# Kernel tuning notes

Measured on AMD Instinct MI355X. Metric: run time of the kernel, lower is better.

The kernel has to match this reference:

```python
import jax, jax.numpy as jnp
import numpy as np

DN = ('NCHW', 'OIHW', 'NCHW')
THRESHOLD = 20   # Broyden iterations (hardcoded in the torch forward)


def conv(x, k):
    return jax.lax.conv_general_dilated(x, k, (1, 1), 'SAME', dimension_numbers=DN)


def _matvec(Us, VTs, v):
    # (-I + Us @ VTs) v ; Us [B,D,K], VTs [B,K,D], v [B,D]
    return -v + jnp.einsum('bdk,bk->bd', Us, jnp.einsum('bkd,bd->bk', VTs, v))


def _rmatvec(Us, VTs, v):
    # v^T (-I + Us @ VTs)
    return -v + jnp.einsum('bk,bkd->bd', jnp.einsum('bd,bdk->bk', v, Us), VTs)


def broyden_solve(g, x0, threshold):
    """Broyden's method with low-rank inverse-Jacobian updates (J^{-1} = -I + Us VTs),
    returning the iterate with the lowest residual norm (as in the DEQ broyden solver)."""
    B, D = x0.shape
    x, gx = x0, g(x0)
    Us = jnp.zeros((B, D, threshold), x0.dtype)
    VTs = jnp.zeros((B, threshold, D), x0.dtype)
    best_x, best_obj = x, jnp.linalg.norm(gx)
    update = gx  # -(-I) gx with empty low-rank part
    for k in range(threshold):
        x_new = x + update
        gx_new = g(x_new)
        dx, dgx = x_new - x, gx_new - gx
        vT = _rmatvec(Us, VTs, dx)                       # [B,D]
        denom = jnp.einsum('bd,bd->b', vT, dgx)[:, None]
        denom = jnp.where(jnp.abs(denom) < 1e-9, 1e-9, denom)
        u = (dx - _matvec(Us, VTs, dgx)) / denom
        Us = Us.at[:, :, k].set(u)
        VTs = VTs.at[:, k, :].set(vT)
        x, gx = x_new, gx_new
        obj = jnp.linalg.norm(gx)
        best_x = jnp.where(obj < best_obj, x, best_x)
        best_obj = jnp.minimum(obj, best_obj)
        update = -_matvec(Us, VTs, gx)
    return best_x


def setup_inputs() -> dict:
    key = jax.random.key(0)
    k1, k2, k3, k4 = jax.random.split(key, 4)
    B, Cin, Cout, H, W = 16, 64, 128, 32, 32
    x = jax.random.normal(k1, (B, Cin, H, W), jnp.float32)
    # small-norm A so relu(conv(z,A)+...) is a contraction -> equilibrium exists
    A = jax.random.normal(k2, (Cout, Cout, 3, 3), jnp.float32) * 0.02
    U = jax.random.normal(k3, (Cout, Cin, 3, 3), jnp.float32) * 0.05
    b = jax.random.normal(k4, (1, Cout, 1, 1), jnp.float32) * 0.1
    return {'x': x, 'A': A, 'U': U, 'b': b}


def reference(x, A, U, b):
    B, _, H, W = x.shape
    Cout = A.shape[0]
    D = Cout * H * W
    ux = conv(x, U) + b  # input injection, constant over iterations

    def g(zvec):  # residual g(z) = relu(Wz + Ux + b) - z, flattened
        z = zvec.reshape(B, Cout, H, W)
        return (jax.nn.relu(conv(z, A) + ux) - z).reshape(B, D)

    z0 = jnp.zeros((B, D), x.dtype)
    zstar = broyden_solve(g, z0, THRESHOLD).reshape(B, Cout, H, W)
    # final recompute with the equilibrium (the torch code re-runs linear+nonlin)
    zn = jax.nn.relu(conv(zstar, A) + ux)
    return zn
```

## Files before the change

### kernel.cpp

```cpp
#include <hip/hip_runtime.h>

#define NB    16
#define CIN_  64
#define COUT_ 128
#define PLANE_ 1024
#define DDIM  (COUT_*PLANE_)
#define BDTOT ((size_t)NB*DDIM)
#define KMAX  20
#define SMAX  16
#define SEG   (DDIM / SMAX)
#define GRP8  (SEG / 8)
#define CBLK  128
#define PADC  8

typedef short  bfrag __attribute__((ext_vector_type(8)));
typedef float  ffrag __attribute__((ext_vector_type(4)));

__device__ __forceinline__ float bf2f(unsigned short h) {
    return __uint_as_float(((unsigned int)h) << 16);
}
__device__ __forceinline__ unsigned short f2bf(float f) {
    unsigned int u = __float_as_uint(f);
    u = (u + 0x7FFFu + ((u >> 16) & 1u)) >> 16;
    return (unsigned short)u;
}
__device__ __forceinline__ void bf2x(unsigned int w, float& lo, float& hi) {
    lo = __uint_as_float(w << 16);
    hi = __uint_as_float(w & 0xffff0000u);
}
__device__ __forceinline__ unsigned int packbf(float lo, float hi) {
    return ((unsigned int)f2bf(hi) << 16) | (unsigned int)f2bf(lo);
}
__device__ __forceinline__ void ub4(ushort4 a, float* f) {
    f[0] = bf2f(a.x); f[1] = bf2f(a.y); f[2] = bf2f(a.z); f[3] = bf2f(a.w);
}
__device__ __forceinline__ ushort4 pk4(const float* f) {
    ushort4 r; r.x = f2bf(f[0]); r.y = f2bf(f[1]); r.z = f2bf(f[2]); r.w = f2bf(f[3]);
    return r;
}
__device__ __forceinline__ void ub8(uint4 a, float* f) {
    bf2x(a.x, f[0], f[1]); bf2x(a.y, f[2], f[3]);
    bf2x(a.z, f[4], f[5]); bf2x(a.w, f[6], f[7]);
}
__device__ __forceinline__ float wred(float v) {
    #pragma unroll
    for (int m = 32; m > 0; m >>= 1) v += __shfl_xor(v, m, 64);
    return v;
}

template<int CIN>
__device__ __forceinline__ void conv_stage_lds(
    const unsigned short* __restrict__ zsrc, unsigned short* lds,
    int hrow, int n, int tid)
{
    const int CP = CIN + PADC;
    const int CH8 = CIN / 8;
    for (int idx = tid; idx < 102 * CH8; idx += 256) {
        int slot = idx / CH8, chunk = idx - slot * CH8;
        int row = slot / 34, pxm = slot - row * 34;
        int h = hrow + row - 1, w = pxm - 1;
        uint4 val = {0u, 0u, 0u, 0u};
        if ((unsigned)h < 32u && (unsigned)w < 32u)
            val = *(const uint4*)(zsrc + ((size_t)n * PLANE_ + h * 32 + w) * CIN + chunk * 8);
        *(uint4*)(lds + (slot)*CP + chunk * 8) = val;
    }
    __syncthreads();
}

template<int CIN>
__device__ __forceinline__ void conv_compute_lds(
    const unsigned short* lds, const unsigned short* __restrict__ Wt,
    int co_base, int col, int quad, ffrag accs[4])
{
    const int CP = CIN + PADC;
    #pragma unroll
    for (int cb = 0; cb < CIN; cb += 32) {
        #pragma unroll
        for (int tap = 0; tap < 9; ++tap) {
            const int dh = tap / 3, dwi = tap % 3;
            const unsigned short* wr0 =
                Wt + ((size_t)tap * COUT_ + co_base + col) * CIN + quad * 8 + cb;
            bfrag a0 = *(const bfrag*)(wr0);
            bfrag a1 = *(const bfrag*)(wr0 + 16 * CIN);
            bfrag b0 = *(const bfrag*)(lds + (dh * 34 + col + dwi) * CP + cb + quad * 8);
            bfrag b1 = *(const bfrag*)(lds + (dh * 34 + col + 16 + dwi) * CP + cb + quad * 8);
            accs[0] = __builtin_amdgcn_mfma_f32_16x16x32_bf16(a0, b0, accs[0], 0, 0, 0);
            accs[1] = __builtin_amdgcn_mfma_f32_16x16x32_bf16(a0, b1, accs[1], 0, 0, 0);
            accs[2] = __builtin_amdgcn_mfma_f32_16x16x32_bf16(a1, b0, accs[2], 0, 0, 0);
            accs[3] = __builtin_amdgcn_mfma_f32_16x16x32_bf16(a1, b1, accs[3], 0, 0, 0);
        }
    }
}

__global__ __launch_bounds__(256) void conv_ux_kernel(
    const unsigned short* __restrict__ xinb, const unsigned short* __restrict__ WU,
    const float* __restrict__ bias, float* __restrict__ ux,
    unsigned short* __restrict__ uxb)
{
    __shared__ unsigned short lds[3 * 34 * (CIN_ + PADC)];
    const int hrow = blockIdx.x, n = blockIdx.y;
    const int tid = threadIdx.x, lane = tid & 63, wv = tid >> 6;
    const int col = lane & 15, quad = lane >> 4;
    conv_stage_lds<CIN_>(xinb, lds, hrow, n, tid);
    ffrag accs[4] = {{0.f,0.f,0.f,0.f},{0.f,0.f,0.f,0.f},{0.f,0.f,0.f,0.f},{0.f,0.f,0.f,0.f}};
    conv_compute_lds<CIN_>(lds, WU, wv * 32, col, quad, accs);
    #pragma unroll
    for (int f = 0; f < 4; ++f) {
        const int mt = f >> 1, nt = f & 1;
        const int co = wv * 32 + mt * 16 + quad * 4;
        const int px = hrow * 32 + nt * 16 + col;
        const size_t o = ((size_t)n * PLANE_ + px) * COUT_ + co;
        float4 bv = *(const float4*)(bias + co);
        float r[4] = {accs[f][0] + bv.x, accs[f][1] + bv.y, accs[f][2] + bv.z, accs[f][3] + bv.w};
        *(float4*)(ux + o) = make_float4(r[0], r[1], r[2], r[3]);
        *(ushort4*)(uxb + o) = pk4(r);
    }
}

__global__ __launch_bounds__(256) void conv_bro_kernel(
    const unsigned short* __restrict__ zb, const unsigned short* __restrict__ WA,
    const unsigned short* __restrict__ uxb, const float* __restrict__ xv,
    unsigned short* gxb,
    const unsigned short* __restrict__ updb,
    unsigned short* __restrict__ dgxb,
    float* __restrict__ cparts)
{
    __shared__ unsigned short lds[3 * 34 * (COUT_ + PADC)];
    const int hrow = blockIdx.x, n = blockIdx.y;
    const int tid = threadIdx.x, lane = tid & 63, wv = tid >> 6;
    const int col = lane & 15, quad = lane >> 4;
    conv_stage_lds<COUT_>(zb, lds, hrow, n, tid);
    ffrag accs[4] = {{0.f,0.f,0.f,0.f},{0.f,0.f,0.f,0.f},{0.f,0.f,0.f,0.f},{0.f,0.f,0.f,0.f}};
    conv_compute_lds<COUT_>(lds, WA, wv * 32, col, quad, accs);

    float s0 = 0.f, s1 = 0.f, s2 = 0.f, s3 = 0.f, s4 = 0.f, s5 = 0.f;
    #pragma unroll
    for (int f = 0; f < 4; ++f) {
        const int mt = f >> 1, nt = f & 1;
        const int co = wv * 32 + mt * 16 + quad * 4;
        const int px = hrow * 32 + nt * 16 + col;
        const size_t o = ((size_t)n * PLANE_ + px) * COUT_ + co;
        float uxv[4], gov[4], udv[4];
        ub4(*(const ushort4*)(uxb + o), uxv);
        ub4(*(const ushort4*)(gxb + o), gov);
        ub4(*(const ushort4*)(updb + o), udv);
        float4 xc = *(const float4*)(xv + o);
        float g[4], dgv[4];
        #pragma unroll
        for (int r = 0; r < 4; ++r) {
            float tv = accs[f][r] + uxv[r];
            tv = tv > 0.f ? tv : 0.f;
            g[r] = tv - (&xc.x)[r];
            dgv[r] = g[r] - gov[r];
            s0 += udv[r] * dgv[r];
            s1 += udv[r] * g[r];
            s2 += g[r] * g[r];
            s3 += udv[r] * udv[r];
            s4 += dgv[r] * dgv[r];
            s5 += dgv[r] * g[r];
        }
        *(ushort4*)(gxb + o)  = pk4(g);
        *(ushort4*)(dgxb + o) = pk4(dgv);
    }
    s0 = wred(s0); s1 = wred(s1); s2 = wred(s2);
    s3 = wred(s3); s4 = wred(s4); s5 = wred(s5);
    if (lane == 0) {
        const int blk = hrow * 4 + wv;
        cparts[((size_t)0 * NB + n) * CBLK + blk] = s0;
        cparts[((size_t)1 * NB + n) * CBLK + blk] = s1;
        cparts[((size_t)2 * NB + n) * CBLK + blk] = s2;
        cparts[((size_t)3 * NB + n) * CBLK + blk] = s3;
        cparts[((size_t)4 * NB + n) * CBLK + blk] = s4;
        cparts[((size_t)5 * NB + n) * CBLK + blk] = s5;
    }
}

__global__ __launch_bounds__(256) void conv_final_kernel(
    const unsigned short* __restrict__ bestzb, const unsigned short* __restrict__ WA,
    const float* __restrict__ ux, float* __restrict__ out)
{
    __shared__ unsigned short lds[3 * 34 * (COUT_ + PADC)];
    const int hrow = blockIdx.x, n = blockIdx.y;
    const int tid = threadIdx.x, lane = tid & 63, wv = tid >> 6;
    const int col = lane & 15, quad = lane >> 4;
    conv_stage_lds<COUT_>(bestzb, lds, hrow, n, tid);
    ffrag accs[4] = {{0.f,0.f,0.f,0.f},{0.f,0.f,0.f,0.f},{0.f,0.f,0.f,0.f},{0.f,0.f,0.f,0.f}};
    conv_compute_lds<COUT_>(lds, WA, wv * 32, col, quad, accs);
    #pragma unroll
    for (int f = 0; f < 4; ++f) {
        const int mt = f >> 1, nt = f & 1;
        const int co = wv * 32 + mt * 16 + quad * 4;
        const int px = hrow * 32 + nt * 16 + col;
        const size_t o = ((size_t)n * PLANE_ + px) * COUT_ + co;
        float4 uv = *(const float4*)(ux + o);
        #pragma unroll
        for (int r = 0; r < 4; ++r) {
            float t = accs[f][r] + (&uv.x)[r];
            out[((size_t)n * COUT_ + co + r) * PLANE_ + px] = t > 0.f ? t : 0.f;
        }
    }
}

#define NWA (9 * 128 * 128)
#define NWU (9 * 128 * 64)
__global__ __launch_bounds__(256) void prep_w_kernel(
    const float* __restrict__ A, const float* __restrict__ U,
    unsigned short* __restrict__ WA, unsigned short* __restrict__ WU)
{
    int idx = blockIdx.x * 256 + threadIdx.x;
    if (idx < NWA) {
        int tap = idx / (128 * 128), r = idx % (128 * 128);
        int co = r >> 7, ci = r & 127;
        WA[idx] = f2bf(A[(co * 128 + ci) * 9 + tap]);
    } else if (idx < NWA + NWU) {
        int j = idx - NWA;
        int tap = j / (128 * 64), r = j % (128 * 64);
        int co = r >> 6, ci = r & 63;
        WU[j] = f2bf(U[(co * 64 + ci) * 9 + tap]);
    }
}

__global__ __launch_bounds__(256) void prep_xin_kernel(
    const float* __restrict__ x, unsigned short* __restrict__ xb)
{
    int idx = blockIdx.x * 256 + threadIdx.x;
    int n = idx >> 16, r = idx & 65535;
    int px = r >> 6, ci = r & 63;
    xb[idx] = f2bf(x[(n * 64 + ci) * 1024 + px]);
}

__global__ __launch_bounds__(256) void fill0_kernel(float* __restrict__ a)
{
    size_t i = ((size_t)blockIdx.x * 256 + threadIdx.x) * 4;
    *(float4*)(a + i) = make_float4(0.f, 0.f, 0.f, 0.f);
}

__global__ __launch_bounds__(256) void ew_init_kernel(
    const float* __restrict__ ux, unsigned short* __restrict__ gxb,
    unsigned short* __restrict__ updb, float* __restrict__ xv,
    unsigned short* __restrict__ zb, float* __restrict__ objinit)
{
    const int tid = threadIdx.x;
    size_t i = ((size_t)blockIdx.x * 256 + tid) * 8;
    float rr[8];
    float ob = 0.f;
    #pragma unroll
    for (int h = 0; h < 2; ++h) {
        float4 u = *(const float4*)(ux + i + h * 4);
        #pragma unroll
        for (int r = 0; r < 4; ++r) {
            float v = (&u.x)[r];
            v = v > 0.f ? v : 0.f;
            v = bf2f(f2bf(v));
            rr[h*4+r] = v;
            ob += v * v;
        }
    }
    uint4 m = {packbf(rr[0],rr[1]), packbf(rr[2],rr[3]), packbf(rr[4],rr[5]), packbf(rr[6],rr[7])};
    *(uint4*)(gxb  + i) = m;
    *(uint4*)(updb + i) = m;
    *(uint4*)(zb   + i) = m;
    #pragma unroll
    for (int h = 0; h < 2; ++h)
        *(float4*)(xv + i + h * 4) = make_float4(rr[h*4+0], rr[h*4+1], rr[h*4+2], rr[h*4+3]);

    __shared__ float so[256];
    so[tid] = ob;
    __syncthreads();
    for (int s = 128; s > 0; s >>= 1) {
        if (tid < s) so[tid] += so[tid + s];
        __syncthreads();
    }
    if (tid == 0) objinit[blockIdx.x] = so[0];
}

__global__ __launch_bounds__(256) void dots_kernel(
    const unsigned short* __restrict__ Us, const unsigned short* __restrict__ VTs,
    const unsigned short* __restrict__ dgxb,
    float* __restrict__ tparts, int k)
{
    const int b = blockIdx.x, y = blockIdx.y, s = blockIdx.z;
    const int tid = threadIdx.x;
    const size_t segbase = (size_t)b * DDIM + (size_t)s * SEG;
    const unsigned short* M = (y < k) ? (VTs + (size_t)y * BDTOT)
                                      : (Us + (size_t)(y - k) * BDTOT);
    const uint4* m8 = (const uint4*)(M + segbase);
    const uint4* d8 = (const uint4*)(dgxb + segbase);
    float s0 = 0.f;
    #pragma unroll
    for (int it = 0; it < GRP8 / 256; ++it) {
        int g = it * 256 + tid;
        float mv[8], dv[8];
        ub8(m8[g], mv); ub8(d8[g], dv);
        #pragma unroll
        for (int j = 0; j < 8; ++j) s0 = fmaf(mv[j], dv[j], s0);
    }
    __shared__ float r0[256];
    r0[tid] = s0;
    __syncthreads();
    for (int st = 128; st > 0; st >>= 1) {
        if (tid < st) r0[tid] += r0[tid + st];
        __syncthreads();
    }
    if (tid == 0) tparts[((size_t)y * NB + b) * SMAX + s] = r0[0];
}

__global__ __launch_bounds__(256) void pass2_kernel(
    unsigned short* __restrict__ Us, unsigned short* __restrict__ VTs,
    unsigned short* updb,
    const unsigned short* __restrict__ dgxb, const unsigned short* __restrict__ gxb,
    float* xv, unsigned short* __restrict__ zb, unsigned short* __restrict__ bestzb,
    const float* __restrict__ tparts, const float* __restrict__ cparts,
    const float* __restrict__ objinit,
    const float* __restrict__ parr_r, float* __restrict__ parr_w,
    const float* __restrict__ tp_r, float* __restrict__ tp_w,
    const float* __restrict__ hp_r, float* __restrict__ hp_w,
    float* __restrict__ UU, float* __restrict__ obj_arr, int k)
{
    const int b = blockIdx.y;
    const int bx = blockIdx.x;
    const int tid = threadIdx.x;
    const int lane = tid & 63, wv = tid >> 6;

    __shared__ float sq[KMAX], st[KMAX], sp[KMAX], sr[KMAX], sh[KMAX], UUk[KMAX];
    __shared__ float sS[5];
    __shared__ float sden, sc, sflag, sobj, srk;
    __shared__ float red[256];

    {
        float o = 0.f;
        const float* OB = cparts + (size_t)2 * NB * CBLK;
        for (int j = tid; j < NB * CBLK; j += 256) o += OB[j];
        red[tid] = o;
        __syncthreads();
        for (int s = 128; s > 0; s >>= 1) {
            if (tid < s) red[tid] += red[tid + s];
            __syncthreads();
        }
        if (tid == 0) sobj = red[0];
        __syncthreads();
    }
    float obj0 = 0.f;
    if (k == 0) {
        float o = 0.f;
        for (int j = tid; j < 1024; j += 256) o += objinit[j];
        red[tid] = o;
        __syncthreads();
        for (int s = 128; s > 0; s >>= 1) {
            if (tid < s) red[tid] += red[tid + s];
            __syncthreads();
        }
        obj0 = red[0];
        __syncthreads();
    }

    if (tid < k) {
        float qv = 0.f, rv = 0.f;
        #pragma unroll
        for (int s = 0; s < SMAX; ++s) {
            qv += tparts[((size_t)tid * NB + b) * SMAX + s];
            rv += tparts[((size_t)(k + tid) * NB + b) * SMAX + s];
        }
        sq[tid] = qv; sr[tid] = rv;
        st[tid] = qv + tp_r[b * KMAX + tid];
        sh[tid] = rv + hp_r[b * KMAX + tid];
        sp[tid] = parr_r[b * KMAX + tid];
    }
    if (wv == 1) {
        float a0 = 0.f, a1 = 0.f;
        for (int j = lane; j < CBLK; j += 64) {
            a0 += cparts[((size_t)0 * NB + b) * CBLK + j];
            a1 += cparts[((size_t)3 * NB + b) * CBLK + j];
        }
        a0 = wred(a0); a1 = wred(a1);
        if (lane == 0) { sS[0] = a0; sS[2] = a1; }
    } else if (wv == 2) {
        float a0 = 0.f, a1 = 0.f;
        for (int j = lane; j < CBLK; j += 64) {
            a0 += cparts[((size_t)1 * NB + b) * CBLK + j];
            a1 += cparts[((size_t)4 * NB + b) * CBLK + j];
        }
        a0 = wred(a0); a1 = wred(a1);
        if (lane == 0) { sS[1] = a0; sS[3] = a1; }
    } else if (wv == 3) {
        float a0 = 0.f;
        for (int j = lane; j < CBLK; j += 64)
            a0 += cparts[((size_t)5 * NB + b) * CBLK + j];
        a0 = wred(a0);
        if (lane == 0) sS[4] = a0;
    }
    __syncthreads();

    if (tid == 0) {
        float pq = 0.f, pt = 0.f;
        for (int i = 0; i < k; ++i) { pq += sp[i] * sq[i]; pt += sp[i] * st[i]; }
        float den = -sS[0] + pq;
        if (fabsf(den) < 1e-9f) den = 1e-9f;
        sden = den;
        float rk = -sS[1] + pt;
        srk = rk;
        sc = rk / den;
        float best;
        if (k == 0) best = obj0;
        else {
            best = obj_arr[0];
            for (int j = 1; j <= k; ++j) best = fminf(best, obj_arr[j]);
        }
        sflag = (sobj < best) ? 1.f : 0.f;
    }
    __syncthreads();

    const size_t base = (size_t)b * DDIM + ((size_t)bx * 256 + tid) * 8;
    float xd[8], dg[8], gv[8];
    ub8(*(const uint4*)(updb + base), xd);
    ub8(*(const uint4*)(dgxb + base), dg);
    ub8(*(const uint4*)(gxb  + base), gv);

    float S1[8], S2[8], SV[8];
    #pragma unroll
    for (int j = 0; j < 8; ++j) { S1[j] = 0.f; S2[j] = 0.f; SV[j] = 0.f; }

    int i = 0;
    for (; i + 1 < k; i += 2) {
        uint4 ru0 = *(const uint4*)(Us  + (size_t)i * BDTOT + base);
        uint4 rv0 = *(const uint4*)(VTs + (size_t)i * BDTOT + base);
        uint4 ru1 = *(const uint4*)(Us  + (size_t)(i + 1) * BDTOT + base);
        uint4 rv1 = *(const uint4*)(VTs + (size_t)(i + 1) * BDTOT + base);
        float u0[8], v0[8], u1[8], v1[8];
        ub8(ru0, u0); ub8(rv0, v0); ub8(ru1, u1); ub8(rv1, v1);
        float q0 = sq[i], t0 = st[i], p0 = sp[i];
        float q1 = sq[i+1], t1 = st[i+1], p1 = sp[i+1];
        #pragma unroll
        for (int j = 0; j < 8; ++j) {
            S1[j] = fmaf(q0, u0[j], fmaf(q1, u1[j], S1[j]));
            S2[j] = fmaf(t0, u0[j], fmaf(t1, u1[j], S2[j]));
            SV[j] = fmaf(p0, v0[j], fmaf(p1, v1[j], SV[j]));
        }
    }
    if (i < k) {
        float uvals[8], vvals[8];
        ub8(*(const uint4*)(Us  + (size_t)i * BDTOT + base), uvals);
        ub8(*(const uint4*)(VTs + (size_t)i * BDTOT + base), vvals);
        float qi = sq[i], ti = st[i], pi = sp[i];
        #pragma unroll
        for (int j = 0; j < 8; ++j) {
            S1[j] = fmaf(qi, uvals[j], S1[j]);
            S2[j] = fmaf(ti, uvals[j], S2[j]);
            SV[j] = fmaf(pi, vvals[j], SV[j]);
        }
    }

    float vk[8], uk[8], up[8];
    #pragma unroll
    for (int j = 0; j < 8; ++j) {
        vk[j] = -xd[j] + SV[j];
        uk[j] = (xd[j] + dg[j] - S1[j]) / sden;
        up[j] = gv[j] - sc * (xd[j] + dg[j]) - S2[j] + sc * S1[j];
    }
    uint4 vks = {packbf(vk[0],vk[1]), packbf(vk[2],vk[3]), packbf(vk[4],vk[5]), packbf(vk[6],vk[7])};
    uint4 uks = {packbf(uk[0],uk[1]), packbf(uk[2],uk[3]), packbf(uk[4],uk[5]), packbf(uk[6],uk[7])};
    *(uint4*)(VTs + (size_t)k * BDTOT + base) = vks;
    *(uint4*)(Us  + (size_t)k * BDTOT + base) = uks;

    uint4 upw = {packbf(up[0],up[1]), packbf(up[2],up[3]), packbf(up[4],up[5]), packbf(up[6],up[7])};
    *(uint4*)(updb + base) = upw;
    float upr[8];
    ub8(upw, upr);

    float xc[8];
    #pragma unroll
    for (int h = 0; h < 2; ++h) {
        float4 a = *(const float4*)(xv + base + h * 4);
        xc[h*4+0]=a.x; xc[h*4+1]=a.y; xc[h*4+2]=a.z; xc[h*4+3]=a.w;
    }
    if (sflag != 0.f) {
        uint4 bz = {packbf(xc[0],xc[1]), packbf(xc[2],xc[3]),
                    packbf(xc[4],xc[5]), packbf(xc[6],xc[7])};
        *(uint4*)(bestzb + base) = bz;
    }
    float xn[8];
    #pragma unroll
    for (int j = 0; j < 8; ++j) xn[j] = xc[j] + upr[j];
    #pragma unroll
    for (int h = 0; h < 2; ++h)
        *(float4*)(xv + base + h * 4) = make_float4(xn[h*4+0], xn[h*4+1], xn[h*4+2], xn[h*4+3]);
    uint4 zn = {packbf(xn[0],xn[1]), packbf(xn[2],xn[3]), packbf(xn[4],xn[5]), packbf(xn[6],xn[7])};
    *(uint4*)(zb + base) = zn;

    if (bx == 0) {
        const float den = sden, cc = sc;
        if (tid < k) {
            float acc = sp[tid] + sr[tid];
            for (int j = 0; j < k; ++j)
                acc -= sq[j] * UU[((size_t)b * KMAX + j) * KMAX + tid];
            UUk[tid] = acc / den;
        }
        __syncthreads();
        if (tid == 0) {
            float ww = sS[2] + 2.f * sS[0] + sS[3];
            float wg = sS[1] + sS[4];
            float sumqh = 0.f, sumqpr = 0.f, sumqU = 0.f;
            for (int j = 0; j < k; ++j) {
                sumqh += sq[j] * sh[j];
                sumqpr += sq[j] * (sp[j] + sr[j]);
                sumqU += sq[j] * UUk[j];
            }
            float ug = (wg - sumqh) / den;
            float uw = (ww - sumqpr) / den;
            float UUkk = (uw - sumqU) / den;
            for (int l = 0; l < k; ++l) {
                UU[((size_t)b * KMAX + k) * KMAX + l] = UUk[l];
                UU[((size_t)b * KMAX + l) * KMAX + k] = UUk[l];
            }
            UU[((size_t)b * KMAX + k) * KMAX + k] = UUkk;
            float acc = ug - cc * uw;
            for (int l = 0; l < k; ++l)
                acc -= (st[l] - cc * sq[l]) * UUk[l];
            parr_w[b * KMAX + k] = acc;
            tp_w[b * KMAX + k] = srk;
            hp_w[b * KMAX + k] = ug;
            if (b == 0) {
                if (k == 0) obj_arr[0] = obj0;
                obj_arr[k + 1] = sobj;
            }
        }
        if (tid < k) {
            float acc = sh[tid] - cc * (sp[tid] + sr[tid]);
            for (int l = 0; l < k; ++l)
                acc -= (st[l] - cc * sq[l]) * UU[((size_t)b * KMAX + tid) * KMAX + l];
            parr_w[b * KMAX + tid] = acc;
            tp_w[b * KMAX + tid] = st[tid];
            hp_w[b * KMAX + tid] = sh[tid];
        }
    }
}

__global__ __launch_bounds__(256) void bestfinal_kernel(
    const float* __restrict__ cparts, const float* __restrict__ obj_arr,
    const unsigned short* __restrict__ zb, unsigned short* __restrict__ bestzb)
{
    const int tid = threadIdx.x;
    __shared__ float red[256];
    __shared__ float sflag;
    float o = 0.f;
    const float* OB = cparts + (size_t)2 * NB * CBLK;
    for (int j = tid; j < NB * CBLK; j += 256) o += OB[j];
    red[tid] = o;
    __syncthreads();
    for (int s = 128; s > 0; s >>= 1) {
        if (tid < s) red[tid] += red[tid + s];
        __syncthreads();
    }
    if (tid == 0) {
        float best = obj_arr[0];
        for (int j = 1; j < KMAX; ++j) best = fminf(best, obj_arr[j]);
        sflag = (red[0] < best) ? 1.f : 0.f;
    }
    __syncthreads();
    if (sflag == 0.f) return;
    size_t i = ((size_t)blockIdx.x * 256 + tid) * 8;
    *(uint4*)(bestzb + i) = *(const uint4*)(zb + i);
}

extern "C" void kernel_launch(void* const* d_in, const int* in_sizes, int n_in,
                              void* d_out, int out_size, void* d_ws, size_t ws_size,
                              hipStream_t stream)
{
    (void)in_sizes; (void)n_in; (void)out_size; (void)ws_size;
    const float* x  = (const float*)d_in[0];
    const float* A  = (const float*)d_in[1];
    const float* U  = (const float*)d_in[2];
    const float* bb = (const float*)d_in[3];
    float* out = (float*)d_out;

    char* w = (char*)d_ws;
    size_t off = 0;
    auto alloc = [&](size_t bytes) -> void* {
        void* pp = (void*)(w + off);
        off += (bytes + 255) & ~(size_t)255;
        return pp;
    };
    const size_t BDB  = BDTOT * sizeof(float);
    const size_t BDH  = BDTOT * 2;
    float* ux    = (float*)alloc(BDB);
    float* xv    = (float*)alloc(BDB);
    unsigned short* uxb    = (unsigned short*)alloc(BDH);
    unsigned short* gxb    = (unsigned short*)alloc(BDH);
    unsigned short* updb   = (unsigned short*)alloc(BDH);
    unsigned short* dgxb   = (unsigned short*)alloc(BDH);
    unsigned short* zb     = (unsigned short*)alloc(BDH);
    unsigned short* bestzb = (unsigned short*)alloc(BDH);
    unsigned short* xinb   = (unsigned short*)alloc((size_t)NB * PLANE_ * CIN_ * 2);
    unsigned short* WA     = (unsigned short*)alloc((size_t)NWA * 2);
    unsigned short* WU     = (unsigned short*)alloc((size_t)NWU * 2);
    unsigned short* Us  = (unsigned short*)alloc((size_t)KMAX * BDTOT * 2);
    unsigned short* VTs = (unsigned short*)alloc((size_t)KMAX * BDTOT * 2);
    float* cparts = (float*)alloc((size_t)6 * NB * CBLK * sizeof(float));
    float* tparts = (float*)alloc((size_t)2 * KMAX * NB * SMAX * sizeof(float));
    float* objinit= (float*)alloc(1024 * sizeof(float));
    float* parr0 = (float*)alloc(NB * KMAX * sizeof(float));
    float* parr1 = (float*)alloc(NB * KMAX * sizeof(float));
    float* tp0   = (float*)alloc(NB * KMAX * sizeof(float));
    float* tp1   = (float*)alloc(NB * KMAX * sizeof(float));
    float* hp0   = (float*)alloc(NB * KMAX * sizeof(float));
    float* hp1   = (float*)alloc(NB * KMAX * sizeof(float));
    float* UU    = (float*)alloc((size_t)NB * KMAX * KMAX * sizeof(float));
    float* obj_arr = (float*)alloc((KMAX + 1) * sizeof(float));

    const dim3 CG(32, NB);
    const int I8WG = (int)(BDTOT / (256 * 8));

    prep_w_kernel<<<(NWA + NWU + 255) / 256, 256, 0, stream>>>(A, U, WA, WU);
    prep_xin_kernel<<<(NB * PLANE_ * CIN_) / 256, 256, 0, stream>>>(x, xinb);
    fill0_kernel<<<(int)(BDH / (256 * 16)), 256, 0, stream>>>((float*)bestzb);

    conv_ux_kernel<<<CG, 256, 0, stream>>>(xinb, WU, bb, ux, uxb);
    ew_init_kernel<<<I8WG, 256, 0, stream>>>(ux, gxb, updb, xv, zb, objinit);

    float* parr[2] = {parr0, parr1};
    float* tp[2]   = {tp0, tp1};
    float* hp[2]   = {hp0, hp1};
    for (int k = 0; k < KMAX; ++k) {
        conv_bro_kernel<<<CG, 256, 0, stream>>>(zb, WA, uxb, xv, gxb, updb, dgxb, cparts);
        if (k < KMAX - 1) {
            if (k > 0)
                dots_kernel<<<dim3(NB, 2 * k, SMAX), 256, 0, stream>>>(
                    Us, VTs, dgxb, tparts, k);
            pass2_kernel<<<dim3(DDIM / 2048, NB), 256, 0, stream>>>(
                Us, VTs, updb, dgxb, gxb, xv, zb, bestzb,
                tparts, cparts, objinit,
                parr[k & 1], parr[(k + 1) & 1],
                tp[k & 1], tp[(k + 1) & 1],
                hp[k & 1], hp[(k + 1) & 1],
                UU, obj_arr, k);
        } else {
            bestfinal_kernel<<<I8WG, 256, 0, stream>>>(cparts, obj_arr, zb, bestzb);
        }
    }

    conv_final_kernel<<<CG, 256, 0, stream>>>(bestzb, WA, ux, out);
}
```

Measured before the change: 1.349 ms.

## Restructure dots kernel to reuse dgx across rows and deepen pass2 unroll

The dots kernel now uses a fixed grid of 8 row-groups. Each block loads its 32-element dgx slice into registers once and loops over multiple Us/VTs rows, two at a time. Reductions switch from a shared-memory tree to wave reductions plus a 4-entry combine. This cuts redundant dgx reads and the number of blocks, at the cost of more per-thread serial work and extra syncs. The pass2 low-rank accumulation loop is unrolled by 4 with loads batched up front, and launch bounds now request occupancy of 4.

```diff
diff --git a/kernel.cpp b/kernel.cpp
--- a/kernel.cpp
+++ b/kernel.cpp
@@ -9,7 +9,7 @@
 #define KMAX  20
 #define SMAX  16
 #define SEG   (DDIM / SMAX)
-#define GRP8  (SEG / 8)
+#define GRPY  8
 #define CBLK  128
 #define PADC  8
 
@@ -274,38 +274,72 @@
     if (tid == 0) objinit[blockIdx.x] = so[0];
 }
 
-__global__ __launch_bounds__(256) void dots_kernel(
+__global__ __launch_bounds__(256, 4) void dots_kernel(
     const unsigned short* __restrict__ Us, const unsigned short* __restrict__ VTs,
     const unsigned short* __restrict__ dgxb,
     float* __restrict__ tparts, int k)
 {
-    const int b = blockIdx.x, y = blockIdx.y, s = blockIdx.z;
-    const int tid = threadIdx.x;
-    const size_t segbase = (size_t)b * DDIM + (size_t)s * SEG;
-    const unsigned short* M = (y < k) ? (VTs + (size_t)y * BDTOT)
-                                      : (Us + (size_t)(y - k) * BDTOT);
-    const uint4* m8 = (const uint4*)(M + segbase);
-    const uint4* d8 = (const uint4*)(dgxb + segbase);
-    float s0 = 0.f;
-    #pragma unroll
-    for (int it = 0; it < GRP8 / 256; ++it) {
-        int g = it * 256 + tid;
-        float mv[8], dv[8];
-        ub8(m8[g], mv); ub8(d8[g], dv);
-        #pragma unroll
-        for (int j = 0; j < 8; ++j) s0 = fmaf(mv[j], dv[j], s0);
-    }
-    __shared__ float r0[256];
-    r0[tid] = s0;
-    __syncthreads();
-    for (int st = 128; st > 0; st >>= 1) {
-        if (tid < st) r0[tid] += r0[tid + st];
-        __syncthreads();
-    }
-    if (tid == 0) tparts[((size_t)y * NB + b) * SMAX + s] = r0[0];
-}
-
-__global__ __launch_bounds__(256) void pass2_kernel(
+    const int b = blockIdx.x, grp = blockIdx.y, s = blockIdx.z;
+    const int tid = threadIdx.x, lane = tid & 63, wv = tid >> 6;
+    const size_t segoff = (size_t)b * DDIM + (size_t)s * SEG + (size_t)tid * 32;
+
+    float dv[32];
+    {
+        const uint4* d4 = (const uint4*)(dgxb + segoff);
+        uint4 r0 = d4[0], r1 = d4[1], r2 = d4[2], r3 = d4[3];
+        ub8(r0, dv); ub8(r1, dv + 8); ub8(r2, dv + 16); ub8(r3, dv + 24);
+    }
+    __shared__ float pl[4];
+
+    auto rowptr = [&](int row) -> const uint4* {
+        const unsigned short* M = (row < k) ? (VTs + (size_t)row * BDTOT)
+                                            : (Us + (size_t)(row - k) * BDTOT);
+        return (const uint4*)(M + segoff);
+    };
+
+    int row = grp;
+    for (; row + GRPY < 2 * k; row += 2 * GRPY) {
+        const uint4* m0 = rowptr(row);
+        const uint4* m1 = rowptr(row + GRPY);
+        uint4 a0 = m0[0], a1 = m0[1], a2 = m0[2], a3 = m0[3];
+        uint4 c0 = m1[0], c1 = m1[1], c2 = m1[2], c3 = m1[3];
+        float acc0 = 0.f, acc1 = 0.f;
+        float mv[8];
+        ub8(a0, mv); for (int j = 0; j < 8; ++j) acc0 = fmaf(mv[j], dv[j], acc0);
+        ub8(a1, mv); for (int j = 0; j < 8; ++j) acc0 = fmaf(mv[j], dv[8 + j], acc0);
+        ub8(a2, mv); for (int j = 0; j < 8; ++j) acc0 = fmaf(mv[j], dv[16 + j], acc0);
+        ub8(a3, mv); for (int j = 0; j < 8; ++j) acc0 = fmaf(mv[j], dv[24 + j], acc0);
+        ub8(c0, mv); for (int j = 0; j < 8; ++j) acc1 = fmaf(mv[j], dv[j], acc1);
+        ub8(c1, mv); for (int j = 0; j < 8; ++j) acc1 = fmaf(mv[j], dv[8 + j], acc1);
+        ub8(c2, mv); for (int j = 0; j < 8; ++j) acc1 = fmaf(mv[j], dv[16 + j], acc1);
+        ub8(c3, mv); for (int j = 0; j < 8; ++j) acc1 = fmaf(mv[j], dv[24 + j], acc1);
+        acc0 = wred(acc0); acc1 = wred(acc1);
+        if (lane == 0) pl[wv] = acc0;
+        __syncthreads();
+        if (tid == 0) tparts[((size_t)row * NB + b) * SMAX + s] = pl[0] + pl[1] + pl[2] + pl[3];
+        __syncthreads();
+        if (lane == 0) pl[wv] = acc1;
+        __syncthreads();
+        if (tid == 0) tparts[((size_t)(row + GRPY) * NB + b) * SMAX + s] = pl[0] + pl[1] + pl[2] + pl[3];
+        __syncthreads();
+    }
+    if (row < 2 * k) {
+        const uint4* m0 = rowptr(row);
+        uint4 a0 = m0[0], a1 = m0[1], a2 = m0[2], a3 = m0[3];
+        float acc0 = 0.f;
+        float mv[8];
+        ub8(a0, mv); for (int j = 0; j < 8; ++j) acc0 = fmaf(mv[j], dv[j], acc0);
+        ub8(a1, mv); for (int j = 0; j < 8; ++j) acc0 = fmaf(mv[j], dv[8 + j], acc0);
+        ub8(a2, mv); for (int j = 0; j < 8; ++j) acc0 = fmaf(mv[j], dv[16 + j], acc0);
+        ub8(a3, mv); for (int j = 0; j < 8; ++j) acc0 = fmaf(mv[j], dv[24 + j], acc0);
+        acc0 = wred(acc0);
+        if (lane == 0) pl[wv] = acc0;
+        __syncthreads();
+        if (tid == 0) tparts[((size_t)row * NB + b) * SMAX + s] = pl[0] + pl[1] + pl[2] + pl[3];
+    }
+}
+
+__global__ __launch_bounds__(256, 4) void pass2_kernel(
     unsigned short* __restrict__ Us, unsigned short* __restrict__ VTs,
     unsigned short* updb,
     const unsigned short* __restrict__ dgxb, const unsigned short* __restrict__ gxb,
@@ -421,23 +455,27 @@
     for (int j = 0; j < 8; ++j) { S1[j] = 0.f; S2[j] = 0.f; SV[j] = 0.f; }
 
     int i = 0;
-    for (; i + 1 < k; i += 2) {
-        uint4 ru0 = *(const uint4*)(Us  + (size_t)i * BDTOT + base);
-        uint4 rv0 = *(const uint4*)(VTs + (size_t)i * BDTOT + base);
-        uint4 ru1 = *(const uint4*)(Us  + (size_t)(i + 1) * BDTOT + base);
-        uint4 rv1 = *(const uint4*)(VTs + (size_t)(i + 1) * BDTOT + base);
-        float u0[8], v0[8], u1[8], v1[8];
-        ub8(ru0, u0); ub8(rv0, v0); ub8(ru1, u1); ub8(rv1, v1);
-        float q0 = sq[i], t0 = st[i], p0 = sp[i];
-        float q1 = sq[i+1], t1 = st[i+1], p1 = sp[i+1];
-        #pragma unroll
-        for (int j = 0; j < 8; ++j) {
-            S1[j] = fmaf(q0, u0[j], fmaf(q1, u1[j], S1[j]));
-            S2[j] = fmaf(t0, u0[j], fmaf(t1, u1[j], S2[j]));
-            SV[j] = fmaf(p0, v0[j], fmaf(p1, v1[j], SV[j]));
-        }
-    }
-    if (i < k) {
+    for (; i + 3 < k; i += 4) {
+        uint4 ru[4], rv[4];
+        #pragma unroll
+        for (int m = 0; m < 4; ++m) {
+            ru[m] = *(const uint4*)(Us  + (size_t)(i + m) * BDTOT + base);
+            rv[m] = *(const uint4*)(VTs + (size_t)(i + m) * BDTOT + base);
+        }
+        #pragma unroll
+        for (int m = 0; m < 4; ++m) {
+            float uu[8], vv[8];
+            ub8(ru[m], uu); ub8(rv[m], vv);
+            float qi = sq[i + m], ti = st[i + m], pi = sp[i + m];
+            #pragma unroll
+            for (int j = 0; j < 8; ++j) {
+                S1[j] = fmaf(qi, uu[j], S1[j]);
+                S2[j] = fmaf(ti, uu[j], S2[j]);
+                SV[j] = fmaf(pi, vv[j], SV[j]);
+            }
+        }
+    }
+    for (; i < k; ++i) {
         float uvals[8], vvals[8];
         ub8(*(const uint4*)(Us  + (size_t)i * BDTOT + base), uvals);
         ub8(*(const uint4*)(VTs + (size_t)i * BDTOT + base), vvals);
@@ -624,7 +662,7 @@
         conv_bro_kernel<<<CG, 256, 0, stream>>>(zb, WA, uxb, xv, gxb, updb, dgxb, cparts);
         if (k < KMAX - 1) {
             if (k > 0)
-                dots_kernel<<<dim3(NB, 2 * k, SMAX), 256, 0, stream>>>(
+                dots_kernel<<<dim3(NB, GRPY, SMAX), 256, 0, stream>>>(
                     Us, VTs, dgxb, tparts, k);
             pass2_kernel<<<dim3(DDIM / 2048, NB), 256, 0, stream>>>(
                 Us, VTs, updb, dgxb, gxb, xv, zb, bestzb,
```

Result: no change. 1.368 ms (+1.4%).

## Compute two output rows per conv block and fuse U/V dot products

Applied to the files above, without the earlier changes.

The conv kernels now use 512-thread blocks that stage four input rows in LDS and compute two output rows, so adjacent rows share their halo loads and the grid is halved. The dots kernel now computes the VTs·dgx and Us·dgx dot products in one block, reading dgx once for both instead of launching separate y-slices. The cost is more LDS per block and fewer blocks in the conv grids, which may reduce occupancy.

```diff
diff --git a/kernel.cpp b/kernel.cpp
--- a/kernel.cpp
+++ b/kernel.cpp
@@ -49,16 +49,16 @@
 }
 
 template<int CIN>
-__device__ __forceinline__ void conv_stage_lds(
+__device__ __forceinline__ void conv_stage_lds4(
     const unsigned short* __restrict__ zsrc, unsigned short* lds,
-    int hrow, int n, int tid)
+    int hr0, int n, int tid)
 {
     const int CP = CIN + PADC;
     const int CH8 = CIN / 8;
-    for (int idx = tid; idx < 102 * CH8; idx += 256) {
+    for (int idx = tid; idx < 136 * CH8; idx += 512) {
         int slot = idx / CH8, chunk = idx - slot * CH8;
         int row = slot / 34, pxm = slot - row * 34;
-        int h = hrow + row - 1, w = pxm - 1;
+        int h = hr0 + row - 1, w = pxm - 1;
         uint4 val = {0u, 0u, 0u, 0u};
         if ((unsigned)h < 32u && (unsigned)w < 32u)
             val = *(const uint4*)(zsrc + ((size_t)n * PLANE_ + h * 32 + w) * CIN + chunk * 8);
@@ -92,22 +92,25 @@
     }
 }
 
-__global__ __launch_bounds__(256) void conv_ux_kernel(
+__global__ __launch_bounds__(512) void conv_ux_kernel(
     const unsigned short* __restrict__ xinb, const unsigned short* __restrict__ WU,
     const float* __restrict__ bias, float* __restrict__ ux,
     unsigned short* __restrict__ uxb)
 {
-    __shared__ unsigned short lds[3 * 34 * (CIN_ + PADC)];
-    const int hrow = blockIdx.x, n = blockIdx.y;
+    __shared__ unsigned short lds[4 * 34 * (CIN_ + PADC)];
+    const int hr0 = blockIdx.x * 2, n = blockIdx.y;
     const int tid = threadIdx.x, lane = tid & 63, wv = tid >> 6;
+    const int rloc = wv >> 2, coT = wv & 3;
     const int col = lane & 15, quad = lane >> 4;
-    conv_stage_lds<CIN_>(xinb, lds, hrow, n, tid);
+    conv_stage_lds4<CIN_>(xinb, lds, hr0, n, tid);
+    const unsigned short* ldsw = lds + rloc * 34 * (CIN_ + PADC);
     ffrag accs[4] = {{0.f,0.f,0.f,0.f},{0.f,0.f,0.f,0.f},{0.f,0.f,0.f,0.f},{0.f,0.f,0.f,0.f}};
-    conv_compute_lds<CIN_>(lds, WU, wv * 32, col, quad, accs);
+    conv_compute_lds<CIN_>(ldsw, WU, coT * 32, col, quad, accs);
+    const int hrow = hr0 + rloc;
     #pragma unroll
     for (int f = 0; f < 4; ++f) {
         const int mt = f >> 1, nt = f & 1;
-        const int co = wv * 32 + mt * 16 + quad * 4;
+        const int co = coT * 32 + mt * 16 + quad * 4;
         const int px = hrow * 32 + nt * 16 + col;
         const size_t o = ((size_t)n * PLANE_ + px) * COUT_ + co;
         float4 bv = *(const float4*)(bias + co);
@@ -117,7 +120,7 @@
     }
 }
 
-__global__ __launch_bounds__(256) void conv_bro_kernel(
+__global__ __launch_bounds__(512) void conv_bro_kernel(
     const unsigned short* __restrict__ zb, const unsigned short* __restrict__ WA,
     const unsigned short* __restrict__ uxb, const float* __restrict__ xv,
     unsigned short* gxb,
@@ -125,19 +128,22 @@
     unsigned short* __restrict__ dgxb,
     float* __restrict__ cparts)
 {
-    __shared__ unsigned short lds[3 * 34 * (COUT_ + PADC)];
-    const int hrow = blockIdx.x, n = blockIdx.y;
+    __shared__ unsigned short lds[4 * 34 * (COUT_ + PADC)];
+    const int hr0 = blockIdx.x * 2, n = blockIdx.y;
     const int tid = threadIdx.x, lane = tid & 63, wv = tid >> 6;
+    const int rloc = wv >> 2, coT = wv & 3;
     const int col = lane & 15, quad = lane >> 4;
-    conv_stage_lds<COUT_>(zb, lds, hrow, n, tid);
+    conv_stage_lds4<COUT_>(zb, lds, hr0, n, tid);
+    const unsigned short* ldsw = lds + rloc * 34 * (COUT_ + PADC);
     ffrag accs[4] = {{0.f,0.f,0.f,0.f},{0.f,0.f,0.f,0.f},{0.f,0.f,0.f,0.f},{0.f,0.f,0.f,0.f}};
-    conv_compute_lds<COUT_>(lds, WA, wv * 32, col, quad, accs);
-
+    conv_compute_lds<COUT_>(ldsw, WA, coT * 32, col, quad, accs);
+
+    const int hrow = hr0 + rloc;
     float s0 = 0.f, s1 = 0.f, s2 = 0.f, s3 = 0.f, s4 = 0.f, s5 = 0.f;
     #pragma unroll
     for (int f = 0; f < 4; ++f) {
         const int mt = f >> 1, nt = f & 1;
-        const int co = wv * 32 + mt * 16 + quad * 4;
+        const int co = coT * 32 + mt * 16 + quad * 4;
         const int px = hrow * 32 + nt * 16 + col;
         const size_t o = ((size_t)n * PLANE_ + px) * COUT_ + co;
         float uxv[4], gov[4], udv[4];
@@ -165,7 +171,7 @@
     s0 = wred(s0); s1 = wred(s1); s2 = wred(s2);
     s3 = wred(s3); s4 = wred(s4); s5 = wred(s5);
     if (lane == 0) {
-        const int blk = hrow * 4 + wv;
+        const int blk = hrow * 4 + coT;
         cparts[((size_t)0 * NB + n) * CBLK + blk] = s0;
         cparts[((size_t)1 * NB + n) * CBLK + blk] = s1;
         cparts[((size_t)2 * NB + n) * CBLK + blk] = s2;
@@ -175,21 +181,24 @@
     }
 }
 
-__global__ __launch_bounds__(256) void conv_final_kernel(
+__global__ __launch_bounds__(512) void conv_final_kernel(
     const unsigned short* __restrict__ bestzb, const unsigned short* __restrict__ WA,
     const float* __restrict__ ux, float* __restrict__ out)
 {
-    __shared__ unsigned short lds[3 * 34 * (COUT_ + PADC)];
-    const int hrow = blockIdx.x, n = blockIdx.y;
+    __shared__ unsigned short lds[4 * 34 * (COUT_ + PADC)];
+    const int hr0 = blockIdx.x * 2, n = blockIdx.y;
     const int tid = threadIdx.x, lane = tid & 63, wv = tid >> 6;
+    const int rloc = wv >> 2, coT = wv & 3;
     const int col = lane & 15, quad = lane >> 4;
-    conv_stage_lds<COUT_>(bestzb, lds, hrow, n, tid);
+    conv_stage_lds4<COUT_>(bestzb, lds, hr0, n, tid);
+    const unsigned short* ldsw = lds + rloc * 34 * (COUT_ + PADC);
     ffrag accs[4] = {{0.f,0.f,0.f,0.f},{0.f,0.f,0.f,0.f},{0.f,0.f,0.f,0.f},{0.f,0.f,0.f,0.f}};
-    conv_compute_lds<COUT_>(lds, WA, wv * 32, col, quad, accs);
+    conv_compute_lds<COUT_>(ldsw, WA, coT * 32, col, quad, accs);
+    const int hrow = hr0 + rloc;
     #pragma unroll
     for (int f = 0; f < 4; ++f) {
         const int mt = f >> 1, nt = f & 1;
-        const int co = wv * 32 + mt * 16 + quad * 4;
+        const int co = coT * 32 + mt * 16 + quad * 4;
         const int px = hrow * 32 + nt * 16 + col;
         const size_t o = ((size_t)n * PLANE_ + px) * COUT_ + co;
         float4 uv = *(const float4*)(ux + o);
@@ -279,30 +288,35 @@
     const unsigned short* __restrict__ dgxb,
     float* __restrict__ tparts, int k)
 {
-    const int b = blockIdx.x, y = blockIdx.y, s = blockIdx.z;
+    const int b = blockIdx.x, i = blockIdx.y, s = blockIdx.z;
     const int tid = threadIdx.x;
     const size_t segbase = (size_t)b * DDIM + (size_t)s * SEG;
-    const unsigned short* M = (y < k) ? (VTs + (size_t)y * BDTOT)
-                                      : (Us + (size_t)(y - k) * BDTOT);
-    const uint4* m8 = (const uint4*)(M + segbase);
+    const uint4* v8 = (const uint4*)(VTs + (size_t)i * BDTOT + segbase);
+    const uint4* u8 = (const uint4*)(Us + (size_t)i * BDTOT + segbase);
     const uint4* d8 = (const uint4*)(dgxb + segbase);
-    float s0 = 0.f;
+    float s0 = 0.f, s1 = 0.f;
     #pragma unroll
     for (int it = 0; it < GRP8 / 256; ++it) {
         int g = it * 256 + tid;
-        float mv[8], dv[8];
-        ub8(m8[g], mv); ub8(d8[g], dv);
-        #pragma unroll
-        for (int j = 0; j < 8; ++j) s0 = fmaf(mv[j], dv[j], s0);
-    }
-    __shared__ float r0[256];
-    r0[tid] = s0;
+        float vv[8], uu[8], dv[8];
+        ub8(v8[g], vv); ub8(u8[g], uu); ub8(d8[g], dv);
+        #pragma unroll
+        for (int j = 0; j < 8; ++j) {
+            s0 = fmaf(vv[j], dv[j], s0);
+            s1 = fmaf(uu[j], dv[j], s1);
+        }
+    }
+    __shared__ float r0[256], r1[256];
+    r0[tid] = s0; r1[tid] = s1;
     __syncthreads();
     for (int st = 128; st > 0; st >>= 1) {
-        if (tid < st) r0[tid] += r0[tid + st];
-        __syncthreads();
-    }
-    if (tid == 0) tparts[((size_t)y * NB + b) * SMAX + s] = r0[0];
+        if (tid < st) { r0[tid] += r0[tid + st]; r1[tid] += r1[tid + st]; }
+        __syncthreads();
+    }
+    if (tid == 0) {
+        tparts[((size_t)i * NB + b) * SMAX + s] = r0[0];
+        tparts[((size_t)(k + i) * NB + b) * SMAX + s] = r1[0];
+    }
 }
 
 __global__ __launch_bounds__(256) void pass2_kernel(
@@ -607,24 +621,24 @@
     float* UU    = (float*)alloc((size_t)NB * KMAX * KMAX * sizeof(float));
     float* obj_arr = (float*)alloc((KMAX + 1) * sizeof(float));
 
-    const dim3 CG(32, NB);
+    const dim3 CG2(16, NB);
     const int I8WG = (int)(BDTOT / (256 * 8));
 
     prep_w_kernel<<<(NWA + NWU + 255) / 256, 256, 0, stream>>>(A, U, WA, WU);
     prep_xin_kernel<<<(NB * PLANE_ * CIN_) / 256, 256, 0, stream>>>(x, xinb);
     fill0_kernel<<<(int)(BDH / (256 * 16)), 256, 0, stream>>>((float*)bestzb);
 
-    conv_ux_kernel<<<CG, 256, 0, stream>>>(xinb, WU, bb, ux, uxb);
+    conv_ux_kernel<<<CG2, 512, 0, stream>>>(xinb, WU, bb, ux, uxb);
     ew_init_kernel<<<I8WG, 256, 0, stream>>>(ux, gxb, updb, xv, zb, objinit);
 
     float* parr[2] = {parr0, parr1};
     float* tp[2]   = {tp0, tp1};
     float* hp[2]   = {hp0, hp1};
     for (int k = 0; k < KMAX; ++k) {
-        conv_bro_kernel<<<CG, 256, 0, stream>>>(zb, WA, uxb, xv, gxb, updb, dgxb, cparts);
+        conv_bro_kernel<<<CG2, 512, 0, stream>>>(zb, WA, uxb, xv, gxb, updb, dgxb, cparts);
         if (k < KMAX - 1) {
             if (k > 0)
-                dots_kernel<<<dim3(NB, 2 * k, SMAX), 256, 0, stream>>>(
+                dots_kernel<<<dim3(NB, k, SMAX), 256, 0, stream>>>(
                     Us, VTs, dgxb, tparts, k);
             pass2_kernel<<<dim3(DDIM / 2048, NB), 256, 0, stream>>>(
                 Us, VTs, updb, dgxb, gxb, xv, zb, bestzb,
@@ -638,5 +652,5 @@
         }
     }
 
-    conv_final_kernel<<<CG, 256, 0, stream>>>(bestzb, WA, ux, out);
-}
+    conv_final_kernel<<<CG2, 512, 0, stream>>>(bestzb, WA, ux, out);
+}
```

New measurement: 1.375 ms. No clear change (+1.9%).
